# Kernel optimization log

Hardware: AMD Instinct MI355X
Metric: run time of the kernel (lower is better)

## Reference

```python
import jax, jax.numpy as jnp
import numpy as np
import math

B, T, D, H, FF, L, CS, LC = 8, 512, 512, 8, 2048, 6, 16, 4
DK = D // H
MIN16 = float(np.finfo(np.float16).min)  # masked_fill value used by the module


def _chunk_mask(size, ck, n_left):
    # subsequent_chunk_mask: row i attends [max((i//ck - n_left)*ck, 0), (i//ck + 1)*ck)
    i = np.arange(size)
    j = np.arange(size)
    ci = i // ck
    start = np.maximum((ci - n_left) * ck, 0)
    end = (ci + 1) * ck
    return (j[None, :] >= start[:, None]) & (j[None, :] < end[:, None])


def setup_inputs() -> dict:
    key = jax.random.key(0)
    ks = jax.random.split(key, 16)
    s = 0.02
    rn = lambda k, shp: jax.random.normal(k, shp, jnp.float32) * s
    xs = jax.random.normal(ks[0], (B, T, D), jnp.float32)
    # RelPositionalEncoding sinusoidal table
    pos = np.arange(T, dtype=np.float32)[:, None]
    div = np.exp(np.arange(0, D, 2, dtype=np.float32) * (-math.log(10000.0) / D))
    pe = np.zeros((T, D), np.float32)
    pe[:, 0::2] = np.sin(pos * div)
    pe[:, 1::2] = np.cos(pos * div)
    pos_emb = jnp.asarray(pe)[None]  # (1, T, D)
    mask = jnp.asarray(_chunk_mask(T, CS, LC))[None]  # (1, T, T) bool, True=attend
    return {
        'xs': xs, 'pos_emb': pos_emb, 'mask': mask,
        'Wq': rn(ks[1], (L, D, D)), 'bq': jnp.zeros((L, D)),
        'Wk': rn(ks[2], (L, D, D)), 'bk': jnp.zeros((L, D)),
        'Wv': rn(ks[3], (L, D, D)), 'bv': jnp.zeros((L, D)),
        'Wo': rn(ks[4], (L, D, D)), 'bo': jnp.zeros((L, D)),
        'Wp': rn(ks[5], (L, D, D)),
        'pbu': rn(ks[6], (L, H, DK)), 'pbv': rn(ks[7], (L, H, DK)),
        'ln1_s': jnp.ones((L, D)), 'ln1_b': jnp.zeros((L, D)),
        'ln2_s': jnp.ones((L, D)), 'ln2_b': jnp.zeros((L, D)),
        'W1': rn(ks[8], (L, D, FF)), 'b1': jnp.zeros((L, FF)),
        'W2': rn(ks[9], (L, FF, D)), 'b2': jnp.zeros((L, D)),
        'lnf_s': jnp.ones((D,)), 'lnf_b': jnp.zeros((D,)),
    }


def _ln(x, g, b):
    m = jnp.mean(x, -1, keepdims=True)
    v = jnp.var(x, -1, keepdims=True)
    return (x - m) * jax.lax.rsqrt(v + 1e-5) * g + b


def reference(xs, pos_emb, mask, Wq, bq, Wk, bk, Wv, bv, Wo, bo, Wp, pbu, pbv,
              ln1_s, ln1_b, ln2_s, ln2_b, W1, b1, W2, b2, lnf_s, lnf_b):
    x = xs * math.sqrt(D)          # xscale from positional encoding
    m = mask[:, None, :, :]        # (1,1,T,T)
    scale = 1.0 / math.sqrt(DK)
    for l in range(L):
        h = _ln(x, ln1_s[l], ln1_b[l])
        q = (h @ Wq[l] + bq[l]).reshape(B, T, H, DK)                       # (B,T,H,DK)
        k = (h @ Wk[l] + bk[l]).reshape(B, T, H, DK).transpose(0, 2, 1, 3)  # (B,H,T,DK)
        v = (h @ Wv[l] + bv[l]).reshape(B, T, H, DK).transpose(0, 2, 1, 3)
        p = (pos_emb @ Wp[l]).reshape(T, H, DK).transpose(1, 0, 2)          # (H,T,DK)
        qu = (q + pbu[l]).transpose(0, 2, 1, 3)  # (B,H,T,DK)
        qv = (q + pbv[l]).transpose(0, 2, 1, 3)
        ac = jnp.einsum('bhtd,bhsd->bhts', qu, k)
        bd = jnp.einsum('bhtd,hsd->bhts', qv, p)
        scores = jnp.where(m, (ac + bd) * scale, MIN16)
        attn = jnp.where(m, jax.nn.softmax(scores, axis=-1), 0.0)
        o = jnp.einsum('bhts,bhsd->bthd', attn, v).reshape(B, T, D)
        x = x + o @ Wo[l] + bo[l]
        h2 = _ln(x, ln2_s[l], ln2_b[l])
        x = x + jax.nn.relu(h2 @ W1[l] + b1[l]) @ W2[l] + b2[l]
    return _ln(x, lnf_s, lnf_b)
```

## Files before the change

### kernel.cpp

```cpp
#include <hip/hip_runtime.h>

#define B_ 8
#define T_ 512
#define D_ 512
#define H_ 8
#define FF_ 2048
#define L_ 6
#define CS_ 16
#define LC_ 4
#define DK_ 64
#define MT_ (B_*T_)

typedef unsigned short u16;
typedef __attribute__((ext_vector_type(8))) short bf8_t;
typedef __attribute__((ext_vector_type(4))) float f4_t;

__device__ __forceinline__ float bf2f(u16 u){
  union { unsigned int i; float f; } c; c.i = ((unsigned int)u) << 16; return c.f;
}
__device__ __forceinline__ u16 f2bf(float f){
  union { float f; unsigned int i; } c; c.f = f;
  unsigned int x = c.i;
  return (u16)((x + 0x7FFFu + ((x >> 16) & 1u)) >> 16);
}
__device__ __forceinline__ void ld_lds16(const u16* gp, u16* lp){
  __builtin_amdgcn_global_load_lds((const __attribute__((address_space(1))) void*)gp,
                                   (__attribute__((address_space(3))) void*)lp, 16, 0, 0);
}

__global__ void init_kernel(const float* __restrict__ xs, const float* __restrict__ pe,
                            float* __restrict__ x, u16* __restrict__ pe_bf)
{
  int stride = gridDim.x * blockDim.x;
  int i0 = blockIdx.x * blockDim.x + threadIdx.x;
  const float s = 22.62741699796952f;
  for (int i = i0; i < B_*T_*D_; i += stride) x[i] = xs[i] * s;
  for (int i = i0; i < T_*D_;    i += stride) pe_bf[i] = f2bf(pe[i]);
}

__global__ void transpose_kernel(const float* __restrict__ in, u16* __restrict__ out,
                                 int K, int N)
{
  __shared__ float tile[32][33];
  int l = blockIdx.z;
  const float* src = in + (size_t)l * K * N;
  u16* dst = out + (size_t)l * N * K;
  int n0 = blockIdx.x * 32, k0 = blockIdx.y * 32;
  int tx = threadIdx.x, ty = threadIdx.y;
  #pragma unroll
  for (int i = 0; i < 4; ++i)
    tile[ty + i*8][tx] = src[(size_t)(k0 + ty + i*8) * N + n0 + tx];
  __syncthreads();
  #pragma unroll
  for (int i = 0; i < 4; ++i)
    dst[(size_t)(n0 + ty + i*8) * K + k0 + tx] = f2bf(tile[tx][ty + i*8]);
}

__global__ void transpose_qkv_kernel(const float* __restrict__ Wq, const float* __restrict__ Wk,
                                     const float* __restrict__ Wv, u16* __restrict__ out)
{
  __shared__ float tile[32][33];
  int l = blockIdx.z;
  int n0 = blockIdx.x * 32, k0 = blockIdx.y * 32;
  const float* W = (n0 < 512) ? Wq : (n0 < 1024 ? Wk : Wv);
  int nn0 = n0 & 511;
  const float* src = W + (size_t)l * D_ * D_;
  u16* dst = out + (size_t)l * 3 * D_ * D_;
  int tx = threadIdx.x, ty = threadIdx.y;
  #pragma unroll
  for (int i = 0; i < 4; ++i)
    tile[ty + i*8][tx] = src[(size_t)(k0 + ty + i*8) * D_ + nn0 + tx];
  __syncthreads();
  #pragma unroll
  for (int i = 0; i < 4; ++i)
    dst[(size_t)(n0 + ty + i*8) * D_ + k0 + tx] = f2bf(tile[tx][ty + i*8]);
}

__global__ void pack_bias_kernel(const float* __restrict__ bq, const float* __restrict__ bk,
                                 const float* __restrict__ bv, float* __restrict__ out)
{
  int l = blockIdx.x, t = threadIdx.x;
  out[l*1536 + t]        = bq[l*512 + t];
  out[l*1536 + 512  + t] = bk[l*512 + t];
  out[l*1536 + 1024 + t] = bv[l*512 + t];
}

template <int OUTMODE>
__global__ __launch_bounds__(256) void ln_kernel(const float* __restrict__ x,
    const float* __restrict__ g, const float* __restrict__ b, void* __restrict__ outp)
{
  int lane = threadIdx.x & 63;
  int row  = (blockIdx.x << 2) + (threadIdx.x >> 6);
  const float* xr = x + (size_t)row * D_;
  int d = lane * 8;
  float4 a0 = *(const float4*)(xr + d);
  float4 a1 = *(const float4*)(xr + d + 4);
  float s  = a0.x+a0.y+a0.z+a0.w + a1.x+a1.y+a1.z+a1.w;
  float s2 = a0.x*a0.x+a0.y*a0.y+a0.z*a0.z+a0.w*a0.w
           + a1.x*a1.x+a1.y*a1.y+a1.z*a1.z+a1.w*a1.w;
  #pragma unroll
  for (int off = 32; off > 0; off >>= 1){ s += __shfl_xor(s, off); s2 += __shfl_xor(s2, off); }
  float m  = s * (1.0f / D_);
  float var = s2 * (1.0f / D_) - m*m;
  float rs = rsqrtf(var + 1e-5f);
  float4 g0 = *(const float4*)(g + d), g1 = *(const float4*)(g + d + 4);
  float4 b0 = *(const float4*)(b + d), b1 = *(const float4*)(b + d + 4);
  float o[8];
  o[0]=(a0.x-m)*rs*g0.x+b0.x; o[1]=(a0.y-m)*rs*g0.y+b0.y;
  o[2]=(a0.z-m)*rs*g0.z+b0.z; o[3]=(a0.w-m)*rs*g0.w+b0.w;
  o[4]=(a1.x-m)*rs*g1.x+b1.x; o[5]=(a1.y-m)*rs*g1.y+b1.y;
  o[6]=(a1.z-m)*rs*g1.z+b1.z; o[7]=(a1.w-m)*rs*g1.w+b1.w;
  if (OUTMODE == 1){
    float* outr = (float*)outp + (size_t)row * D_ + d;
    *(float4*)(outr)     = make_float4(o[0],o[1],o[2],o[3]);
    *(float4*)(outr + 4) = make_float4(o[4],o[5],o[6],o[7]);
  } else {
    u16* outr = (u16*)outp + (size_t)row * D_ + d;
    ushort4 w0, w1;
    w0.x=f2bf(o[0]); w0.y=f2bf(o[1]); w0.z=f2bf(o[2]); w0.w=f2bf(o[3]);
    w1.x=f2bf(o[4]); w1.y=f2bf(o[5]); w1.z=f2bf(o[6]); w1.w=f2bf(o[7]);
    *(ushort4*)(outr)     = w0;
    *(ushort4*)(outr + 4) = w1;
  }
}

__global__ __launch_bounds__(256) void mgemm_kernel(
    const u16* __restrict__ A, const u16* __restrict__ Bt,
    const float* __restrict__ bias, const float* __restrict__ resid,
    void* __restrict__ C, int M, int N, int K,
    int relu, int bf16out, size_t wstride, size_t cstride, int kchunk)
{
  constexpr int TN = 64, NT = 2, S = 3;
  size_t coff = 0;
  int kbeg = 0, kend = K;
  if (kchunk > 0){
    kbeg = blockIdx.z * kchunk; kend = kbeg + kchunk;
  } else {
    Bt += (size_t)blockIdx.z * wstride;
    coff = (size_t)blockIdx.z * cstride;
  }

  __shared__ u16 As[3][128 * 32];
  __shared__ u16 Bs[3][TN * 32];

  int tid  = threadIdx.x;
  int wave = tid >> 6, lane = tid & 63;
  int wm = wave >> 1, wn = wave & 1;
  int fm = lane & 15, fq = lane >> 4;

  int m0 = blockIdx.y * 128, n0 = blockIdx.x * TN;

  f4_t acc[4][NT];
  #pragma unroll
  for (int i = 0; i < 4; ++i)
    #pragma unroll
    for (int j = 0; j < NT; ++j) acc[i][j] = (f4_t)0.0f;

  int srow = lane >> 2;
  int selem = (lane & 3) << 3;

  auto stage = [&](int bufi, int k0){
    #pragma unroll
    for (int j = 0; j < 2; ++j){
      int c = wave * 2 + j;
      ld_lds16(A + (size_t)(m0 + c*16 + srow) * K + k0 + selem, &As[bufi][c * 512]);
    }
    ld_lds16(Bt + (size_t)(n0 + wave*16 + srow) * K + k0 + selem, &Bs[bufi][wave * 512]);
  };

  stage(0, kbeg);
  if (kbeg + 32 < kend) stage(1, kbeg + 32);
  int buf = 0;
  for (int k0 = kbeg; k0 < kend; k0 += 32){
    if (k0 + 64 < kend){
      stage((buf + 2) % 3, k0 + 64);
      asm volatile("s_waitcnt vmcnt(%0)" :: "n"(2*S) : "memory");
    } else if (k0 + 32 < kend){
      asm volatile("s_waitcnt vmcnt(%0)" :: "n"(S) : "memory");
    } else {
      asm volatile("s_waitcnt vmcnt(0)" ::: "memory");
    }
    asm volatile("s_barrier" ::: "memory");

    bf8_t af[4], bfr[NT];
    #pragma unroll
    for (int mi = 0; mi < 4; ++mi)
      af[mi] = *(const bf8_t*)&As[buf][(wm*64 + mi*16 + fm) * 32 + fq*8];
    #pragma unroll
    for (int nj = 0; nj < NT; ++nj)
      bfr[nj] = *(const bf8_t*)&Bs[buf][(wn*32 + nj*16 + fm) * 32 + fq*8];
    #pragma unroll
    for (int mi = 0; mi < 4; ++mi)
      #pragma unroll
      for (int nj = 0; nj < NT; ++nj)
        acc[mi][nj] = __builtin_amdgcn_mfma_f32_16x16x32_bf16(af[mi], bfr[nj], acc[mi][nj], 0, 0, 0);

    asm volatile("s_barrier" ::: "memory");
    buf = (buf + 1) % 3;
  }

  int rbase = m0 + wm*64, cbase = n0 + wn*32;
  if (kchunk > 0){
    int addb = (blockIdx.z == 0) && bias;
    #pragma unroll
    for (int mi = 0; mi < 4; ++mi){
      #pragma unroll
      for (int nj = 0; nj < NT; ++nj){
        int col = cbase + nj*16 + fm;
        float bia = addb ? bias[col] : 0.0f;
        #pragma unroll
        for (int r = 0; r < 4; ++r){
          int row = rbase + mi*16 + fq*4 + r;
          atomicAdd((float*)C + (size_t)row * N + col, acc[mi][nj][r] + bia);
        }
      }
    }
  } else {
    #pragma unroll
    for (int mi = 0; mi < 4; ++mi){
      #pragma unroll
      for (int nj = 0; nj < NT; ++nj){
        int col = cbase + nj*16 + fm;
        float bia = bias ? bias[col] : 0.0f;
        #pragma unroll
        for (int r = 0; r < 4; ++r){
          int row = rbase + mi*16 + fq*4 + r;
          size_t idx = coff + (size_t)row * N + col;
          float val = acc[mi][nj][r] + bia;
          if (relu)  val = fmaxf(val, 0.0f);
          if (resid) val += resid[idx];
          if (bf16out) ((u16*)C)[idx] = f2bf(val);
          else         ((float*)C)[idx] = val;
        }
      }
    }
  }
}

__global__ __launch_bounds__(64) void attn_kernel(
    const u16* __restrict__ qkv, const u16* __restrict__ p,
    const float* __restrict__ pbu, const float* __restrict__ pbv,
    u16* __restrict__ o)
{
  int ci = blockIdx.x, h = blockIdx.y, b = blockIdx.z;
  int t0 = ci * CS_;
  int cb = ci - LC_; if (cb < 0) cb = 0;
  int c0 = cb * CS_;
  int ncol = (ci + 1) * CS_ - c0;

  __shared__ u16 smem[15648];
  u16* qu = smem;
  u16* qv = smem + 1024;
  u16* kp = smem + 2048;
  u16* pp = smem + 2048 + 5120;
  float* vf  = (float*)(smem + 2048);
  float* psf = (float*)(smem + 12288);

  int lane = threadIdx.x;
  int fm = lane & 15, fq = lane >> 4;

  const u16* kbase = qkv + ((size_t)(b*T_ + c0)) * 1536 + 512 + h*DK_;
  const u16* pbase = p + (size_t)c0 * D_ + h*DK_;
  int srow8 = lane >> 3, scol = (lane & 7) << 3;
  #pragma unroll
  for (int c = 0; c < 10; ++c){
    ld_lds16(kbase + (size_t)(c*8 + srow8) * 1536 + scol, kp + c*512);
    ld_lds16(pbase + (size_t)(c*8 + srow8) * D_   + scol, pp + c*512);
  }
  const u16* qbase = qkv + ((size_t)(b*T_ + t0)) * 1536 + h*DK_;
  #pragma unroll
  for (int it = 0; it < 4; ++it){
    int i = it*256 + lane*4; int r = i >> 6; int d = i & 63;
    ushort4 w = *(const ushort4*)(qbase + (size_t)r * 1536 + d);
    float4 bu = *(const float4*)(pbu + h*DK_ + d);
    float4 bv = *(const float4*)(pbv + h*DK_ + d);
    ushort4 ou, ov;
    ou.x = f2bf(bf2f(w.x) + bu.x); ou.y = f2bf(bf2f(w.y) + bu.y);
    ou.z = f2bf(bf2f(w.z) + bu.z); ou.w = f2bf(bf2f(w.w) + bu.w);
    ov.x = f2bf(bf2f(w.x) + bv.x); ov.y = f2bf(bf2f(w.y) + bv.y);
    ov.z = f2bf(bf2f(w.z) + bv.z); ov.w = f2bf(bf2f(w.w) + bv.w);
    *(ushort4*)(qu + r*64 + d) = ou;
    *(ushort4*)(qv + r*64 + d) = ov;
  }
  __syncthreads();

  bf8_t au0 = *(const bf8_t*)(qu + fm*64 + fq*8);
  bf8_t au1 = *(const bf8_t*)(qu + fm*64 + 32 + fq*8);
  bf8_t av0 = *(const bf8_t*)(qv + fm*64 + fq*8);
  bf8_t av1 = *(const bf8_t*)(qv + fm*64 + 32 + fq*8);
  f4_t acc[5];
  #pragma unroll
  for (int nt = 0; nt < 5; ++nt) acc[nt] = (f4_t)0.0f;
  #pragma unroll
  for (int nt = 0; nt < 5; ++nt){
    const u16* kr = kp + (nt*16 + fm)*64;
    const u16* pr = pp + (nt*16 + fm)*64;
    bf8_t bk0 = *(const bf8_t*)(kr + fq*8);
    bf8_t bk1 = *(const bf8_t*)(kr + 32 + fq*8);
    bf8_t bp0 = *(const bf8_t*)(pr + fq*8);
    bf8_t bp1 = *(const bf8_t*)(pr + 32 + fq*8);
    f4_t a = acc[nt];
    a = __builtin_amdgcn_mfma_f32_16x16x32_bf16(au0, bk0, a, 0, 0, 0);
    a = __builtin_amdgcn_mfma_f32_16x16x32_bf16(au1, bk1, a, 0, 0, 0);
    a = __builtin_amdgcn_mfma_f32_16x16x32_bf16(av0, bp0, a, 0, 0, 0);
    a = __builtin_amdgcn_mfma_f32_16x16x32_bf16(av1, bp1, a, 0, 0, 0);
    acc[nt] = a;
  }

  const float scale = 0.125f;
  float mx[4], sm[4];
  float e[5][4];
  #pragma unroll
  for (int r = 0; r < 4; ++r) mx[r] = -3.0e38f;
  #pragma unroll
  for (int nt = 0; nt < 5; ++nt){
    bool valid = (nt*16 + fm) < ncol;
    #pragma unroll
    for (int r = 0; r < 4; ++r){
      float v = valid ? acc[nt][r] : -3.0e38f;
      mx[r] = fmaxf(mx[r], v);
    }
  }
  #pragma unroll
  for (int r = 0; r < 4; ++r){
    #pragma unroll
    for (int m = 1; m < 16; m <<= 1) mx[r] = fmaxf(mx[r], __shfl_xor(mx[r], m));
    sm[r] = 0.0f;
  }
  #pragma unroll
  for (int nt = 0; nt < 5; ++nt){
    bool valid = (nt*16 + fm) < ncol;
    #pragma unroll
    for (int r = 0; r < 4; ++r){
      float ev = valid ? __expf((acc[nt][r] - mx[r]) * scale) : 0.0f;
      e[nt][r] = ev; sm[r] += ev;
    }
  }
  #pragma unroll
  for (int r = 0; r < 4; ++r){
    #pragma unroll
    for (int m = 1; m < 16; m <<= 1) sm[r] += __shfl_xor(sm[r], m);
    sm[r] = 1.0f / sm[r];
  }
  #pragma unroll
  for (int nt = 0; nt < 5; ++nt)
    #pragma unroll
    for (int r = 0; r < 4; ++r)
      psf[(fq*4 + r)*105 + nt*16 + fm] = e[nt][r] * sm[r];
  __syncthreads();

  const u16* vbase = qkv + ((size_t)(b*T_ + c0)) * 1536 + 1024 + h*DK_;
  #pragma unroll
  for (int it = 0; it < 20; ++it){
    int i = it*256 + lane*4; int s = i >> 6; int d = i & 63;
    ushort4 w = *(const ushort4*)(vbase + (size_t)s * 1536 + d);
    float4 f; f.x = bf2f(w.x); f.y = bf2f(w.y); f.z = bf2f(w.z); f.w = bf2f(w.w);
    *(float4*)(vf + s*64 + d) = f;
  }
  __syncthreads();

  float oacc[16];
  #pragma unroll
  for (int ii = 0; ii < 16; ++ii) oacc[ii] = 0.0f;
  const float* psr = psf + fm*105;
  const float* vcol = vf + fq*16;
  for (int s = 0; s < 80; ++s){
    float pv = psr[s];
    const float* vr = vcol + s*64;
    float4 v0 = *(const float4*)(vr);
    float4 v1 = *(const float4*)(vr + 4);
    float4 v2 = *(const float4*)(vr + 8);
    float4 v3 = *(const float4*)(vr + 12);
    oacc[0]  += pv*v0.x; oacc[1]  += pv*v0.y; oacc[2]  += pv*v0.z; oacc[3]  += pv*v0.w;
    oacc[4]  += pv*v1.x; oacc[5]  += pv*v1.y; oacc[6]  += pv*v1.z; oacc[7]  += pv*v1.w;
    oacc[8]  += pv*v2.x; oacc[9]  += pv*v2.y; oacc[10] += pv*v2.z; oacc[11] += pv*v2.w;
    oacc[12] += pv*v3.x; oacc[13] += pv*v3.y; oacc[14] += pv*v3.z; oacc[15] += pv*v3.w;
  }
  u16* ob = o + ((size_t)(b*T_ + t0 + fm)) * D_ + h*DK_ + fq*16;
  #pragma unroll
  for (int q4 = 0; q4 < 4; ++q4){
    ushort4 w;
    w.x = f2bf(oacc[q4*4+0]); w.y = f2bf(oacc[q4*4+1]);
    w.z = f2bf(oacc[q4*4+2]); w.w = f2bf(oacc[q4*4+3]);
    *(ushort4*)(ob + q4*4) = w;
  }
}

extern "C" void kernel_launch(void* const* d_in, const int* in_sizes, int n_in,
                              void* d_out, int out_size, void* d_ws, size_t ws_size,
                              hipStream_t stream)
{
  int s0 = (n_in >= 24) ? 0 : -1;
  const float* xs   = (const float*)d_in[0];
  const float* pe   = (const float*)d_in[1];
  const float* Wq   = (const float*)d_in[3  + s0];
  const float* bq   = (const float*)d_in[4  + s0];
  const float* Wk   = (const float*)d_in[5  + s0];
  const float* bk   = (const float*)d_in[6  + s0];
  const float* Wv   = (const float*)d_in[7  + s0];
  const float* bv   = (const float*)d_in[8  + s0];
  const float* Wo   = (const float*)d_in[9  + s0];
  const float* bo   = (const float*)d_in[10 + s0];
  const float* Wp   = (const float*)d_in[11 + s0];
  const float* pbu  = (const float*)d_in[12 + s0];
  const float* pbv  = (const float*)d_in[13 + s0];
  const float* ln1s = (const float*)d_in[14 + s0];
  const float* ln1b = (const float*)d_in[15 + s0];
  const float* ln2s = (const float*)d_in[16 + s0];
  const float* ln2b = (const float*)d_in[17 + s0];
  const float* W1   = (const float*)d_in[18 + s0];
  const float* b1   = (const float*)d_in[19 + s0];
  const float* W2   = (const float*)d_in[20 + s0];
  const float* b2   = (const float*)d_in[21 + s0];
  const float* lnfs = (const float*)d_in[22 + s0];
  const float* lnfb = (const float*)d_in[23 + s0];

  float* ws = (float*)d_ws;
  size_t cur = 0;
  float* x      = ws + cur;            cur += (size_t)MT_*D_;
  u16*   region = (u16*)(ws + cur);    cur += (size_t)MT_*FF_/2;
  u16*   qkv_bf = region;
  u16*   ff_bf  = region;
  u16*   h_bf   = (u16*)(ws + cur);    cur += (size_t)MT_*D_/2;
  u16*   ob_bf  = (u16*)(ws + cur);    cur += (size_t)MT_*D_/2;
  u16*   pe_bf  = (u16*)(ws + cur);    cur += (size_t)T_*D_/2;
  u16*   pbuf   = (u16*)(ws + cur);    cur += (size_t)L_*T_*D_/2;
  u16*   qkvt   = (u16*)(ws + cur);    cur += (size_t)L_*3*D_*D_/2;
  u16*   wot    = (u16*)(ws + cur);    cur += (size_t)L_*D_*D_/2;
  u16*   w1t    = (u16*)(ws + cur);    cur += (size_t)L_*D_*FF_/2;
  u16*   w2t    = (u16*)(ws + cur);    cur += (size_t)L_*FF_*D_/2;
  u16*   wpt    = (u16*)(ws + cur);    cur += (size_t)L_*D_*D_/2;
  float* bqkv   = ws + cur;            cur += (size_t)L_*3*D_;

  dim3 tb(32, 8);
  transpose_qkv_kernel<<<dim3(48, 16, L_), tb, 0, stream>>>(Wq, Wk, Wv, qkvt);
  transpose_kernel<<<dim3(16, 16, L_), tb, 0, stream>>>(Wo, wot, D_, D_);
  transpose_kernel<<<dim3(64, 16, L_), tb, 0, stream>>>(W1, w1t, D_, FF_);
  transpose_kernel<<<dim3(16, 64, L_), tb, 0, stream>>>(W2, w2t, FF_, D_);
  transpose_kernel<<<dim3(16, 16, L_), tb, 0, stream>>>(Wp, wpt, D_, D_);
  pack_bias_kernel<<<dim3(L_), dim3(512), 0, stream>>>(bq, bk, bv, bqkv);
  init_kernel<<<dim3(512), dim3(256), 0, stream>>>(xs, pe, x, pe_bf);

  dim3 blk(256);
  mgemm_kernel<<<dim3(8, 4, L_), blk, 0, stream>>>(
      pe_bf, wpt, nullptr, nullptr, pbuf, T_, D_, D_, 0, 1,
      (size_t)D_*D_, (size_t)T_*D_, 0);

  for (int l = 0; l < L_; ++l){
    ln_kernel<0><<<dim3(MT_/4), blk, 0, stream>>>(x, ln1s + l*D_, ln1b + l*D_, h_bf);
    mgemm_kernel<<<dim3(24, 32, 1), blk, 0, stream>>>(
        h_bf, qkvt + (size_t)l*3*D_*D_, bqkv + l*3*D_, nullptr, qkv_bf,
        MT_, 3*D_, D_, 0, 1, 0, 0, 0);
    attn_kernel<<<dim3(T_/CS_, H_, B_), dim3(64), 0, stream>>>(
        qkv_bf, pbuf + (size_t)l*T_*D_, pbu + l*H_*DK_, pbv + l*H_*DK_, ob_bf);
    mgemm_kernel<<<dim3(8, 32, 2), blk, 0, stream>>>(
        ob_bf, wot + (size_t)l*D_*D_, bo + l*D_, nullptr, x,
        MT_, D_, D_, 0, 0, 0, 0, 256);
    ln_kernel<0><<<dim3(MT_/4), blk, 0, stream>>>(x, ln2s + l*D_, ln2b + l*D_, h_bf);
    mgemm_kernel<<<dim3(32, 32, 1), blk, 0, stream>>>(
        h_bf, w1t + (size_t)l*D_*FF_, b1 + l*FF_, nullptr, ff_bf,
        MT_, FF_, D_, 1, 1, 0, 0, 0);
    mgemm_kernel<<<dim3(8, 32, 4), blk, 0, stream>>>(
        ff_bf, w2t + (size_t)l*FF_*D_, b2 + l*D_, nullptr, x,
        MT_, D_, FF_, 0, 0, 0, 0, 512);
  }
  ln_kernel<1><<<dim3(MT_/4), blk, 0, stream>>>(x, lnfs, lnfb, d_out);
}
```

Before: 971.1 us.

## Fuse FFN up and down projections into one kernel keeping hidden in LDS

```diff
diff --git a/kernel.cpp b/kernel.cpp
--- a/kernel.cpp
+++ b/kernel.cpp
@@ -233,6 +233,81 @@
           else         ((float*)C)[idx] = val;
         }
       }
+    }
+  }
+}
+
+#define FP_ 520
+__global__ __launch_bounds__(256) void ffused_kernel(
+    const u16* __restrict__ h, const u16* __restrict__ w1t, const float* __restrict__ b1,
+    const u16* __restrict__ w2t, const float* __restrict__ b2, float* __restrict__ x)
+{
+  __shared__ u16 hs[16 * FP_];
+  __shared__ u16 ffs[16 * FP_];
+
+  int tid = threadIdx.x;
+  int wave = tid >> 6, lane = tid & 63;
+  int fm = lane & 15, fq = lane >> 4;
+  int m0 = blockIdx.x * 16;
+
+  #pragma unroll
+  for (int it = 0; it < 4; ++it){
+    int idx = it*256 + tid;
+    int row = idx >> 6;
+    int col = (idx & 63) << 3;
+    const u16* src = h + (size_t)(m0 + row) * D_ + col;
+    *(ushort4*)(hs + row*FP_ + col)     = *(const ushort4*)(src);
+    *(ushort4*)(hs + row*FP_ + col + 4) = *(const ushort4*)(src + 4);
+  }
+  __syncthreads();
+
+  f4_t acc2[8];
+  #pragma unroll
+  for (int j = 0; j < 8; ++j) acc2[j] = (f4_t)0.0f;
+
+  for (int nc = 0; nc < 4; ++nc){
+    #pragma unroll
+    for (int nt = 0; nt < 8; ++nt){
+      int ffc0 = nc*512 + wave*128 + nt*16;
+      f4_t c = (f4_t)0.0f;
+      #pragma unroll
+      for (int ks = 0; ks < 16; ++ks){
+        bf8_t af = *(const bf8_t*)(hs + fm*FP_ + ks*32 + fq*8);
+        bf8_t bf = *(const bf8_t*)(w1t + (size_t)(ffc0 + fm)*D_ + ks*32 + fq*8);
+        c = __builtin_amdgcn_mfma_f32_16x16x32_bf16(af, bf, c, 0, 0, 0);
+      }
+      int col = ffc0 + fm;
+      float bia = b1[col];
+      int lcol = wave*128 + nt*16 + fm;
+      #pragma unroll
+      for (int r = 0; r < 4; ++r){
+        float v = fmaxf(c[r] + bia, 0.0f);
+        ffs[(fq*4 + r)*FP_ + lcol] = f2bf(v);
+      }
+    }
+    __syncthreads();
+    #pragma unroll
+    for (int ks = 0; ks < 16; ++ks){
+      bf8_t af = *(const bf8_t*)(ffs + fm*FP_ + ks*32 + fq*8);
+      #pragma unroll
+      for (int nt = 0; nt < 8; ++nt){
+        int ocol = wave*128 + nt*16 + fm;
+        bf8_t bf = *(const bf8_t*)(w2t + (size_t)ocol*FF_ + nc*512 + ks*32 + fq*8);
+        acc2[nt] = __builtin_amdgcn_mfma_f32_16x16x32_bf16(af, bf, acc2[nt], 0, 0, 0);
+      }
+    }
+    __syncthreads();
+  }
+
+  #pragma unroll
+  for (int nt = 0; nt < 8; ++nt){
+    int col = wave*128 + nt*16 + fm;
+    float bia = b2[col];
+    #pragma unroll
+    for (int r = 0; r < 4; ++r){
+      int row = m0 + fq*4 + r;
+      float* px = x + (size_t)row * D_ + col;
+      *px += acc2[nt][r] + bia;
     }
   }
 }
@@ -418,9 +493,7 @@
   float* ws = (float*)d_ws;
   size_t cur = 0;
   float* x      = ws + cur;            cur += (size_t)MT_*D_;
-  u16*   region = (u16*)(ws + cur);    cur += (size_t)MT_*FF_/2;
-  u16*   qkv_bf = region;
-  u16*   ff_bf  = region;
+  u16*   qkv_bf = (u16*)(ws + cur);    cur += (size_t)MT_*3*D_/2;
   u16*   h_bf   = (u16*)(ws + cur);    cur += (size_t)MT_*D_/2;
   u16*   ob_bf  = (u16*)(ws + cur);    cur += (size_t)MT_*D_/2;
   u16*   pe_bf  = (u16*)(ws + cur);    cur += (size_t)T_*D_/2;
@@ -457,12 +530,9 @@
         ob_bf, wot + (size_t)l*D_*D_, bo + l*D_, nullptr, x,
         MT_, D_, D_, 0, 0, 0, 0, 256);
     ln_kernel<0><<<dim3(MT_/4), blk, 0, stream>>>(x, ln2s + l*D_, ln2b + l*D_, h_bf);
-    mgemm_kernel<<<dim3(32, 32, 1), blk, 0, stream>>>(
-        h_bf, w1t + (size_t)l*D_*FF_, b1 + l*FF_, nullptr, ff_bf,
-        MT_, FF_, D_, 1, 1, 0, 0, 0);
-    mgemm_kernel<<<dim3(8, 32, 4), blk, 0, stream>>>(
-        ff_bf, w2t + (size_t)l*FF_*D_, b2 + l*D_, nullptr, x,
-        MT_, D_, FF_, 0, 0, 0, 0, 512);
+    ffused_kernel<<<dim3(MT_/16), blk, 0, stream>>>(
+        h_bf, w1t + (size_t)l*D_*FF_, b1 + l*FF_,
+        w2t + (size_t)l*FF_*D_, b2 + l*D_, x);
   }
   ln_kernel<1><<<dim3(MT_/4), blk, 0, stream>>>(x, lnfs, lnfb, d_out);
 }
```

After: 1.922 ms. 1.98x slower.
